# Kernel optimization log

Measured on AMD Instinct MI355X. Metric: run time of the kernel, lower is better.

Reference implementation:

```python
import jax, jax.numpy as jnp
import numpy as np

M_FUZZ = 2.0        # self.m
EPSILON = 1e-8      # self.Epsilon
MAX_ITER = 25       # self.max_iterion


def setup_inputs() -> dict:
    key = jax.random.key(0)
    k1, k2 = jax.random.split(key)
    data = jax.random.normal(k1, (300000, 64), dtype=jnp.float32)
    u0_raw = jax.random.uniform(k2, (300000, 64), dtype=jnp.float32)
    return {"data": data, "u0_raw": u0_raw, "cluster": 64}


def reference(data, u0_raw, cluster):
    # Fuzzy c-means, faithful to GranularComputing.forward:
    #   iterate: C = center(U); U = update(U, C); C_new = center(U);
    #            stop if ||C_new - C||_F < Epsilon; return C (pre-update center).
    m = M_FUZZ
    p = 2.0 / (m - 1.0)  # exponent in membership update (== 2.0)
    N, D = data.shape

    # initialize_matrix_U: random rows normalized to sum to 1
    U0 = u0_raw / jnp.sum(u0_raw, axis=1, keepdims=True)  # [N, c]

    def center(U):
        Um = U ** m                                        # [N, c]
        num = Um.T @ data                                  # [c, D]
        den = jnp.sum(Um, axis=0)[:, None]                 # [c, 1]
        return num / den

    x2 = jnp.sum(data * data, axis=1, keepdims=True)       # [N, 1]

    def sqdist(C):
        # squared Euclidean distances [N, c] via expansion (no N x c x D tensor)
        c2 = jnp.sum(C * C, axis=1)                        # [c]
        return jnp.maximum(x2 + c2 - 2.0 * (data @ C.T), 0.0)

    def step(carry, _):
        U, C_ret, done = carry
        C = center(U)                                      # [c, D]
        # u_ij = 1 / sum_k (d_ij / d_ik)^p  ==  d_ij^{-p} / sum_k d_ik^{-p}
        w = sqdist(C) ** (-p / 2.0)                        # [N, c]
        U_new = w / jnp.sum(w, axis=1, keepdims=True)
        C_new = center(U_new)
        diff = jnp.sqrt(jnp.sum((C_new - C) ** 2))
        # freeze state after convergence (emulates the early break)
        U_out = jnp.where(done, U, U_new)
        C_out = jnp.where(done, C_ret, C)
        return (U_out, C_out, done | (diff < EPSILON)), None

    C0 = jnp.zeros((cluster, D), dtype=data.dtype)
    (_, V, _), _ = jax.lax.scan(
        step, (U0, C0, jnp.array(False)), None, length=MAX_ITER + 1
    )
    return V  # [cluster, D]
```

## Files before the change

kernel.cpp:

```cpp
#include <hip/hip_runtime.h>


#define DM 64
#define CL 64
#define PARTIAL_STRIDE 4160
#define MAX_ITER 25
#define MAX_BLOCKS 768
#define LDP 72

typedef __attribute__((ext_vector_type(8))) short bf16x8;
typedef __attribute__((ext_vector_type(4))) float f32x4;

__device__ __forceinline__ unsigned f2bf1(float f) {
  unsigned u = __builtin_bit_cast(unsigned, f);
  return (u + 0x7FFFu + ((u >> 16) & 1u)) >> 16;
}
__device__ __forceinline__ unsigned pkbf(float a, float b) {
  return f2bf1(a) | (f2bf1(b) << 16);
}
__device__ __forceinline__ unsigned cvtpk_bf16(float a, float b) {
  unsigned r;
  asm("v_cvt_pk_bf16_f32 %0, %1, %2" : "=v"(r) : "v"(a), "v"(b));
  return r;
}

__device__ __forceinline__ float wave_sum(float v) {
#define DPPADD(ctrl, rmask)                                                  \
  v += __builtin_bit_cast(float, __builtin_amdgcn_update_dpp(                \
           0, __builtin_bit_cast(int, v), ctrl, rmask, 0xf, false));
  DPPADD(0x111, 0xf)
  DPPADD(0x112, 0xf)
  DPPADD(0x114, 0xf)
  DPPADD(0x118, 0xf)
  DPPADD(0x142, 0xa)
  DPPADD(0x143, 0xc)
#undef DPPADD
  return __builtin_bit_cast(
      float, __builtin_amdgcn_readlane(__builtin_bit_cast(int, v), 63));
}

__device__ __forceinline__ float group16_sum(float v) {
#define DPPADD(ctrl)                                                         \
  v += __builtin_bit_cast(float, __builtin_amdgcn_update_dpp(                \
           0, __builtin_bit_cast(int, v), ctrl, 0xf, 0xf, false));
  DPPADD(0xB1)
  DPPADD(0x4E)
  DPPADD(0x141)
  DPPADD(0x140)
#undef DPPADD
  return v;
}

__global__ __launch_bounds__(256)
void fcm_prep(const float* __restrict__ data, float* __restrict__ x2,
              unsigned short* __restrict__ xbf,
              float* __restrict__ diffac, int* __restrict__ done,
              int* __restrict__ ticket, int N) {
  size_t i = (size_t)blockIdx.x * blockDim.x + threadIdx.x;
  if (i == 0) { *diffac = 0.0f; *done = 0; *ticket = 0; }
  size_t nvec = (size_t)N * (DM / 4);
  if (i >= nvec) return;
  float4 v = ((const float4*)data)[i];
  float s = fmaf(v.x, v.x, fmaf(v.y, v.y, fmaf(v.z, v.z, v.w * v.w)));
  float rs = group16_sum(s);
  if ((threadIdx.x & 15) == 0) x2[i >> 4] = rs;
  uint2 pk = {cvtpk_bf16(v.x, v.y), cvtpk_bf16(v.z, v.w)};
  ((uint2*)xbf)[i] = pk;
}

template <bool INIT>
__global__ __launch_bounds__(256, 3)
void fcm_pass(const unsigned short* __restrict__ xbf, const float* __restrict__ x2,
              const float* __restrict__ CU,
              float* __restrict__ partial, const int* __restrict__ done,
              int N, int ntiles) {
  if (!INIT && *done) return;
  __shared__ __align__(16) unsigned short Xb[64 * LDP];
  __shared__ __align__(16) unsigned short XTb[64 * LDP];
  __shared__ __align__(16) unsigned short umT[64 * LDP];
  __shared__ __align__(16) float x2s[64];

  const int tid  = threadIdx.x;
  const int w    = __builtin_amdgcn_readfirstlane(tid >> 6);
  const int col  = tid & 15;
  const int quad = (tid >> 4) & 3;

  bf16x8 cf0[4], cf1[4];
  float c2v[4];
  if (!INIT) {
#pragma unroll
    for (int jt = 0; jt < 4; jt++) {
      const float* crow = CU + (size_t)(16 * jt + col) * DM;
      float4 ca = *(const float4*)(crow + quad * 8);
      float4 cb = *(const float4*)(crow + quad * 8 + 4);
      float4 cc = *(const float4*)(crow + 32 + quad * 8);
      float4 cd = *(const float4*)(crow + 32 + quad * 8 + 4);
      float cp = ca.x*ca.x + ca.y*ca.y + ca.z*ca.z + ca.w*ca.w
               + cb.x*cb.x + cb.y*cb.y + cb.z*cb.z + cb.w*cb.w
               + cc.x*cc.x + cc.y*cc.y + cc.z*cc.z + cc.w*cc.w
               + cd.x*cd.x + cd.y*cd.y + cd.z*cd.z + cd.w*cd.w;
      cp += __shfl_xor(cp, 16, 64);
      cp += __shfl_xor(cp, 32, 64);
      c2v[jt] = cp;
      union { bf16x8 v; unsigned u[4]; } P0, P1;
      P0.u[0] = pkbf(ca.x, ca.y); P0.u[1] = pkbf(ca.z, ca.w);
      P0.u[2] = pkbf(cb.x, cb.y); P0.u[3] = pkbf(cb.z, cb.w);
      P1.u[0] = pkbf(cc.x, cc.y); P1.u[1] = pkbf(cc.z, cc.w);
      P1.u[2] = pkbf(cd.x, cd.y); P1.u[3] = pkbf(cd.z, cd.w);
      cf0[jt] = P0.v; cf1[jt] = P1.v;
    }
  }

  union { bf16x8 v; unsigned u[4]; } ON;
  ON.u[0] = ON.u[1] = ON.u[2] = ON.u[3] = 0x3F803F80u;
  const bf16x8 onesf = ON.v;

  f32x4 D2[4];
#pragma unroll
  for (int dt = 0; dt < 4; dt++) D2[dt] = f32x4{0.f, 0.f, 0.f, 0.f};
  f32x4 Dden = f32x4{0.f, 0.f, 0.f, 0.f};

  const int sp  = tid & 63;
  const int sd0 = (tid >> 6) * 8;
  const unsigned short* gsrc = xbf + (size_t)sp * DM + sd0;
  unsigned short* xw = &Xb[sp * LDP + sd0];
  unsigned short* xt = &XTb[sd0 * LDP + sp];

  for (int t = blockIdx.x; t < ntiles; t += gridDim.x) {
    const int base = t * 64;
    const int np = min(64, N - base);
    __syncthreads();

    {
      bf16x8 v0 = {0, 0, 0, 0, 0, 0, 0, 0};
      bf16x8 v1 = {0, 0, 0, 0, 0, 0, 0, 0};
      if (sp < np) {
        const unsigned short* g = gsrc + (size_t)base * DM;
        v0 = *(const bf16x8*)(g);
        v1 = *(const bf16x8*)(g + 32);
      }
      *(bf16x8*)(void*)xw = v0;
      *(bf16x8*)(void*)(xw + 32) = v1;
#pragma unroll
      for (int k = 0; k < 8; k++) xt[k * LDP] = (unsigned short)v0[k];
#pragma unroll
      for (int k = 0; k < 8; k++) xt[(k + 32) * LDP] = (unsigned short)v1[k];
    }
    if (tid < 64) x2s[tid] = (base + tid < N) ? x2[base + tid] : 0.0f;
    __syncthreads();

    float Wv[4][4];
    if (INIT) {
#pragma unroll
      for (int jt = 0; jt < 4; jt++)
#pragma unroll
        for (int r = 0; r < 4; r++) {
          int pl = 16 * w + quad * 4 + r;
          Wv[jt][r] = (pl < np)
              ? CU[(size_t)(base + pl) * CL + 16 * jt + col] : 0.0f;
        }
    } else {
      bf16x8 a0 = *(const bf16x8*)(const void*)&Xb[(16 * w + col) * LDP + quad * 8];
      bf16x8 a1 = *(const bf16x8*)(const void*)&Xb[(16 * w + col) * LDP + 32 + quad * 8];
      f32x4 x2p = *(const f32x4*)(const void*)&x2s[16 * w + quad * 4];
#pragma unroll
      for (int jt = 0; jt < 4; jt++) {
        f32x4 s = f32x4{0.f, 0.f, 0.f, 0.f};
        s = __builtin_amdgcn_mfma_f32_16x16x32_bf16(a0, cf0[jt], s, 0, 0, 0);
        s = __builtin_amdgcn_mfma_f32_16x16x32_bf16(a1, cf1[jt], s, 0, 0, 0);
#pragma unroll
        for (int r = 0; r < 4; r++) {
          float dist = fmaxf(fmaf(-2.0f, s[r], x2p[r] + c2v[jt]), 0.0f);
          Wv[jt][r] = __builtin_amdgcn_rcpf(dist);
        }
      }
    }

    float rr[4];
#pragma unroll
    for (int r = 0; r < 4; r++) {
      float rs = Wv[0][r] + Wv[1][r] + Wv[2][r] + Wv[3][r];
      rs = group16_sum(rs);
      int pl = 16 * w + quad * 4 + r;
      rr[r] = (pl < np) ? __builtin_amdgcn_rcpf(rs) : 0.0f;
    }

#pragma unroll
    for (int jt = 0; jt < 4; jt++) {
      float u0v = Wv[jt][0] * rr[0], u1v = Wv[jt][1] * rr[1];
      float u2v = Wv[jt][2] * rr[2], u3v = Wv[jt][3] * rr[3];
      uint2 pk = {cvtpk_bf16(u0v * u0v, u1v * u1v),
                  cvtpk_bf16(u2v * u2v, u3v * u3v)};
      *(uint2*)(void*)&umT[(16 * jt + col) * LDP + 16 * w + quad * 4] = pk;
    }
    __syncthreads();

#pragma unroll
    for (int pb = 0; pb < 2; pb++) {
      bf16x8 au = *(const bf16x8*)(const void*)&umT[(16 * w + col) * LDP + pb * 32 + quad * 8];
      Dden = __builtin_amdgcn_mfma_f32_16x16x32_bf16(au, onesf, Dden, 0, 0, 0);
#pragma unroll
      for (int dt = 0; dt < 4; dt++) {
        bf16x8 bx = *(const bf16x8*)(const void*)&XTb[(dt * 16 + col) * LDP + pb * 32 + quad * 8];
        D2[dt] = __builtin_amdgcn_mfma_f32_16x16x32_bf16(au, bx, D2[dt], 0, 0, 0);
      }
    }
  }

  float* pbuf = partial + (size_t)blockIdx.x * PARTIAL_STRIDE;
  if (col == 0) {
    float4 dv = {Dden[0], Dden[1], Dden[2], Dden[3]};
    *(float4*)(void*)&pbuf[CL * DM + 16 * w + quad * 4] = dv;
  }
#pragma unroll
  for (int dt = 0; dt < 4; dt++)
#pragma unroll
    for (int r = 0; r < 4; r++)
      pbuf[(size_t)(16 * w + quad * 4 + r) * DM + dt * 16 + col] = D2[dt][r];
}

__global__ __launch_bounds__(1024, 1)
void fcm_reduce(const float* __restrict__ partial, float* __restrict__ Cnew,
                const float* __restrict__ Cold, float* __restrict__ out,
                float* __restrict__ diffac, int* __restrict__ done,
                int* __restrict__ ticket, int compute_diff, int nb) {
  if (compute_diff && *done) return;
  __shared__ float sm[16 * 64];
  __shared__ float sden[1024];
  __shared__ int lastflag;
  __shared__ float sdiff;
  int j = blockIdx.x;
  int tid = threadIdx.x;
  int d = tid & 63;
  int slice = tid >> 6;
  float s = 0.0f;
  for (int b = slice; b < nb; b += 16)
    s += partial[(size_t)b * PARTIAL_STRIDE + j * DM + d];
  sm[slice * 64 + d] = s;
  float dv = 0.0f;
  for (int b = tid; b < nb; b += 1024)
    dv += partial[(size_t)b * PARTIAL_STRIDE + CL * DM + j];
  sden[tid] = dv;
  __syncthreads();
#pragma unroll
  for (int st = 8; st; st >>= 1) {
    if (slice < st) sm[slice * 64 + d] += sm[(slice + st) * 64 + d];
    __syncthreads();
  }
#pragma unroll
  for (int st = 512; st >= 64; st >>= 1) {
    if (tid < st) sden[tid] += sden[tid + st];
    __syncthreads();
  }
  if (tid < 64) {
    float denj = wave_sum(sden[tid]);
    float c = sm[tid] / denj;
    Cnew[j * DM + tid] = c;
    if (compute_diff) {
      float df = c - Cold[j * DM + tid];
      float tot = wave_sum(df * df);
      if (tid == 0) atomicAdd(diffac, tot);
    }
  }
  if (!compute_diff) return;
  __syncthreads();
  if (tid == 0) {
    __threadfence();
    int t = atomicAdd(ticket, 1);
    lastflag = (t == (int)gridDim.x - 1);
  }
  __syncthreads();
  if (!lastflag) return;
  if (tid == 0) sdiff = atomicAdd(diffac, 0.0f);
  __syncthreads();
  if (sdiff < 1e-16f) {
    for (int i = tid; i < CL * DM; i += 1024) out[i] = Cold[i];
    if (tid == 0) *done = 1;
  }
  if (tid == 0) { *diffac = 0.0f; *ticket = 0; }
}

__global__ void fcm_final(const float* __restrict__ Clast, float* __restrict__ out,
                          const int* __restrict__ done) {
  if (*done) return;
  int i = blockIdx.x * blockDim.x + threadIdx.x;
  if (i < CL * DM) out[i] = Clast[i];
}

extern "C" void kernel_launch(void* const* d_in, const int* in_sizes, int n_in,
                              void* d_out, int out_size, void* d_ws, size_t ws_size,
                              hipStream_t stream) {
  const float* data = (const float*)d_in[0];
  const float* u0   = (const float*)d_in[1];
  float* out = (float*)d_out;
  int N = in_sizes[0] / DM;
  int ntiles = (N + 63) / 64;

  float* ws = (float*)d_ws;
  size_t Noff = ((size_t)N + 15) & ~(size_t)15;
  float* x2 = ws;
  unsigned short* xbf = (unsigned short*)(ws + Noff);
  float* C0 = ws + Noff + (size_t)N * 32;
  float* C1 = C0 + CL * DM;
  float* diffac = C1 + CL * DM;
  int* done = (int*)(diffac + 1);
  int* ticket = (int*)(diffac + 2);
  float* partial = diffac + 16;

  size_t used = Noff + (size_t)N * 32 + 2 * CL * DM + 16;
  size_t avail = (ws_size / 4 > used) ? (ws_size / 4 - used) / PARTIAL_STRIDE : 0;
  int nb = (int)(avail < MAX_BLOCKS ? avail : MAX_BLOCKS);
  if (nb < 1) nb = 1;

  size_t nvec = (size_t)N * (DM / 4);
  hipLaunchKernelGGL(fcm_prep, dim3((unsigned)((nvec + 255) / 256)), dim3(256), 0,
                     stream, data, x2, xbf, diffac, done, ticket, N);
  hipLaunchKernelGGL((fcm_pass<true>), dim3(nb), dim3(256), 0, stream,
                     xbf, x2, u0, partial, done, N, ntiles);
  hipLaunchKernelGGL(fcm_reduce, dim3(64), dim3(1024), 0, stream,
                     partial, C0, C1, out, diffac, done, ticket, 0, nb);

  float* bufs[2] = {C0, C1};
  for (int k = 0; k < MAX_ITER; k++) {
    float* Cc = bufs[k & 1];
    float* Cn = bufs[(k + 1) & 1];
    hipLaunchKernelGGL((fcm_pass<false>), dim3(nb), dim3(256), 0, stream,
                       xbf, x2, Cc, partial, done, N, ntiles);
    hipLaunchKernelGGL(fcm_reduce, dim3(64), dim3(1024), 0, stream,
                       partial, Cn, Cc, out, diffac, done, ticket, 1, nb);
  }
  hipLaunchKernelGGL(fcm_final, dim3(16), dim3(256), 0, stream,
                     bufs[1], out, done);
}
```

Baseline: 387.6 us.

## Software-pipeline tile loads and split center reduction across four blocks per cluster

The pass kernel now double-buffers the X tiles in LDS and prefetches the next tile's bf16 rows and x2 values into registers. The second GEMM for the previous tile is deferred so it overlaps with staging the current tile, which removes one barrier per tile. The reduce kernel is split into 256 blocks of 256 threads, four per cluster. Each block reduces a quarter of the partials and combines them through global atomics with a per-cluster ticket, plus a global ticket for the convergence check. This adds LDS use, which may lower occupancy, and relies on atomic accumulation and self-resetting counters.

```diff
diff --git a/kernel.cpp b/kernel.cpp
--- a/kernel.cpp
+++ b/kernel.cpp
@@ -7,6 +7,7 @@
 #define MAX_ITER 25
 #define MAX_BLOCKS 768
 #define LDP 72
+#define ZACC_SZ 4224
 
 typedef __attribute__((ext_vector_type(8))) short bf16x8;
 typedef __attribute__((ext_vector_type(4))) float f32x4;
@@ -53,11 +54,12 @@
 
 __global__ __launch_bounds__(256)
 void fcm_prep(const float* __restrict__ data, float* __restrict__ x2,
-              unsigned short* __restrict__ xbf,
+              unsigned short* __restrict__ xbf, float* __restrict__ zacc,
               float* __restrict__ diffac, int* __restrict__ done,
               int* __restrict__ ticket, int N) {
   size_t i = (size_t)blockIdx.x * blockDim.x + threadIdx.x;
   if (i == 0) { *diffac = 0.0f; *done = 0; *ticket = 0; }
+  if (i < ZACC_SZ) zacc[i] = 0.0f;
   size_t nvec = (size_t)N * (DM / 4);
   if (i >= nvec) return;
   float4 v = ((const float4*)data)[i];
@@ -75,10 +77,10 @@
               float* __restrict__ partial, const int* __restrict__ done,
               int N, int ntiles) {
   if (!INIT && *done) return;
-  __shared__ __align__(16) unsigned short Xb[64 * LDP];
-  __shared__ __align__(16) unsigned short XTb[64 * LDP];
+  __shared__ __align__(16) unsigned short Xb[2][64 * LDP];
+  __shared__ __align__(16) unsigned short XTb[2][64 * LDP];
   __shared__ __align__(16) unsigned short umT[64 * LDP];
-  __shared__ __align__(16) float x2s[64];
+  __shared__ __align__(16) float x2s[2][64];
 
   const int tid  = threadIdx.x;
   const int w    = __builtin_amdgcn_readfirstlane(tid >> 6);
@@ -123,30 +125,70 @@
   const int sp  = tid & 63;
   const int sd0 = (tid >> 6) * 8;
   const unsigned short* gsrc = xbf + (size_t)sp * DM + sd0;
-  unsigned short* xw = &Xb[sp * LDP + sd0];
-  unsigned short* xt = &XTb[sd0 * LDP + sp];
-
-  for (int t = blockIdx.x; t < ntiles; t += gridDim.x) {
+
+  auto do_gemm2 = [&](int cb) {
+#pragma unroll
+    for (int pb = 0; pb < 2; pb++) {
+      bf16x8 au = *(const bf16x8*)(const void*)&umT[(16 * w + col) * LDP + pb * 32 + quad * 8];
+      Dden = __builtin_amdgcn_mfma_f32_16x16x32_bf16(au, onesf, Dden, 0, 0, 0);
+#pragma unroll
+      for (int dt = 0; dt < 4; dt++) {
+        bf16x8 bx = *(const bf16x8*)(const void*)&XTb[cb][(dt * 16 + col) * LDP + pb * 32 + quad * 8];
+        D2[dt] = __builtin_amdgcn_mfma_f32_16x16x32_bf16(au, bx, D2[dt], 0, 0, 0);
+      }
+    }
+  };
+
+  bf16x8 rv0 = {0, 0, 0, 0, 0, 0, 0, 0};
+  bf16x8 rv1 = {0, 0, 0, 0, 0, 0, 0, 0};
+  float rx2 = 0.0f;
+  {
+    int t0 = blockIdx.x;
+    if (t0 < ntiles) {
+      int base = t0 * 64;
+      int np = min(64, N - base);
+      if (sp < np) {
+        const unsigned short* g = gsrc + (size_t)base * DM;
+        rv0 = *(const bf16x8*)(g);
+        rv1 = *(const bf16x8*)(g + 32);
+      }
+      if (tid < 64 && base + tid < N) rx2 = x2[base + tid];
+    }
+  }
+
+  int c = 0;
+  int it = 0;
+  for (int t = blockIdx.x; t < ntiles; t += gridDim.x, ++it) {
     const int base = t * 64;
     const int np = min(64, N - base);
     __syncthreads();
 
+    if (it > 0) do_gemm2(c ^ 1);
+
+    *(bf16x8*)(void*)&Xb[c][sp * LDP + sd0] = rv0;
+    *(bf16x8*)(void*)&Xb[c][sp * LDP + sd0 + 32] = rv1;
+#pragma unroll
+    for (int k = 0; k < 8; k++) XTb[c][(sd0 + k) * LDP + sp] = (unsigned short)rv0[k];
+#pragma unroll
+    for (int k = 0; k < 8; k++) XTb[c][(sd0 + 32 + k) * LDP + sp] = (unsigned short)rv1[k];
+    if (tid < 64) x2s[c][tid] = rx2;
+
     {
-      bf16x8 v0 = {0, 0, 0, 0, 0, 0, 0, 0};
-      bf16x8 v1 = {0, 0, 0, 0, 0, 0, 0, 0};
-      if (sp < np) {
-        const unsigned short* g = gsrc + (size_t)base * DM;
-        v0 = *(const bf16x8*)(g);
-        v1 = *(const bf16x8*)(g + 32);
+      int tn = t + gridDim.x;
+      rv0 = bf16x8{0, 0, 0, 0, 0, 0, 0, 0};
+      rv1 = bf16x8{0, 0, 0, 0, 0, 0, 0, 0};
+      rx2 = 0.0f;
+      if (tn < ntiles) {
+        int nbase = tn * 64;
+        int nnp = min(64, N - nbase);
+        if (sp < nnp) {
+          const unsigned short* g = gsrc + (size_t)nbase * DM;
+          rv0 = *(const bf16x8*)(g);
+          rv1 = *(const bf16x8*)(g + 32);
+        }
+        if (tid < 64 && nbase + tid < N) rx2 = x2[nbase + tid];
       }
-      *(bf16x8*)(void*)xw = v0;
-      *(bf16x8*)(void*)(xw + 32) = v1;
-#pragma unroll
-      for (int k = 0; k < 8; k++) xt[k * LDP] = (unsigned short)v0[k];
-#pragma unroll
-      for (int k = 0; k < 8; k++) xt[(k + 32) * LDP] = (unsigned short)v1[k];
-    }
-    if (tid < 64) x2s[tid] = (base + tid < N) ? x2[base + tid] : 0.0f;
+    }
     __syncthreads();
 
     float Wv[4][4];
@@ -160,9 +202,9 @@
               ? CU[(size_t)(base + pl) * CL + 16 * jt + col] : 0.0f;
         }
     } else {
-      bf16x8 a0 = *(const bf16x8*)(const void*)&Xb[(16 * w + col) * LDP + quad * 8];
-      bf16x8 a1 = *(const bf16x8*)(const void*)&Xb[(16 * w + col) * LDP + 32 + quad * 8];
-      f32x4 x2p = *(const f32x4*)(const void*)&x2s[16 * w + quad * 4];
+      bf16x8 a0 = *(const bf16x8*)(const void*)&Xb[c][(16 * w + col) * LDP + quad * 8];
+      bf16x8 a1 = *(const bf16x8*)(const void*)&Xb[c][(16 * w + col) * LDP + 32 + quad * 8];
+      f32x4 x2p = *(const f32x4*)(const void*)&x2s[c][16 * w + quad * 4];
 #pragma unroll
       for (int jt = 0; jt < 4; jt++) {
         f32x4 s = f32x4{0.f, 0.f, 0.f, 0.f};
@@ -193,18 +235,12 @@
                   cvtpk_bf16(u2v * u2v, u3v * u3v)};
       *(uint2*)(void*)&umT[(16 * jt + col) * LDP + 16 * w + quad * 4] = pk;
     }
+    c ^= 1;
+  }
+
+  if (it > 0) {
     __syncthreads();
-
-#pragma unroll
-    for (int pb = 0; pb < 2; pb++) {
-      bf16x8 au = *(const bf16x8*)(const void*)&umT[(16 * w + col) * LDP + pb * 32 + quad * 8];
-      Dden = __builtin_amdgcn_mfma_f32_16x16x32_bf16(au, onesf, Dden, 0, 0, 0);
-#pragma unroll
-      for (int dt = 0; dt < 4; dt++) {
-        bf16x8 bx = *(const bf16x8*)(const void*)&XTb[(dt * 16 + col) * LDP + pb * 32 + quad * 8];
-        D2[dt] = __builtin_amdgcn_mfma_f32_16x16x32_bf16(au, bx, D2[dt], 0, 0, 0);
-      }
-    }
+    do_gemm2(c ^ 1);
   }
 
   float* pbuf = partial + (size_t)blockIdx.x * PARTIAL_STRIDE;
@@ -219,62 +255,69 @@
       pbuf[(size_t)(16 * w + quad * 4 + r) * DM + dt * 16 + col] = D2[dt][r];
 }
 
-__global__ __launch_bounds__(1024, 1)
+__global__ __launch_bounds__(256)
 void fcm_reduce(const float* __restrict__ partial, float* __restrict__ Cnew,
                 const float* __restrict__ Cold, float* __restrict__ out,
+                float* __restrict__ Cacc, float* __restrict__ Dacc,
+                int* __restrict__ jtick,
                 float* __restrict__ diffac, int* __restrict__ done,
                 int* __restrict__ ticket, int compute_diff, int nb) {
   if (compute_diff && *done) return;
-  __shared__ float sm[16 * 64];
-  __shared__ float sden[1024];
+  __shared__ float red[4][64];
   __shared__ int lastflag;
-  __shared__ float sdiff;
-  int j = blockIdx.x;
-  int tid = threadIdx.x;
-  int d = tid & 63;
-  int slice = tid >> 6;
+  __shared__ float sdv;
+  const int tid = threadIdx.x;
+  const int j = blockIdx.x >> 2;
+  const int q = blockIdx.x & 3;
+  const int nbq = nb >> 2;
+  const int i0 = q * nbq;
+  const int iend = (q == 3) ? nb : i0 + nbq;
+  const int d = tid & 63;
+  const int slice = tid >> 6;
+
   float s = 0.0f;
-  for (int b = slice; b < nb; b += 16)
-    s += partial[(size_t)b * PARTIAL_STRIDE + j * DM + d];
-  sm[slice * 64 + d] = s;
-  float dv = 0.0f;
-  for (int b = tid; b < nb; b += 1024)
-    dv += partial[(size_t)b * PARTIAL_STRIDE + CL * DM + j];
-  sden[tid] = dv;
-  __syncthreads();
-#pragma unroll
-  for (int st = 8; st; st >>= 1) {
-    if (slice < st) sm[slice * 64 + d] += sm[(slice + st) * 64 + d];
-    __syncthreads();
-  }
-#pragma unroll
-  for (int st = 512; st >= 64; st >>= 1) {
-    if (tid < st) sden[tid] += sden[tid + st];
-    __syncthreads();
-  }
+  for (int i = i0 + slice; i < iend; i += 4)
+    s += partial[(size_t)i * PARTIAL_STRIDE + j * DM + d];
+  red[slice][d] = s;
+  __syncthreads();
   if (tid < 64) {
-    float denj = wave_sum(sden[tid]);
-    float c = sm[tid] / denj;
-    Cnew[j * DM + tid] = c;
+    float ss = red[0][d] + red[1][d] + red[2][d] + red[3][d];
+    atomicAdd(&Cacc[j * DM + d], ss);
+    float dv = 0.0f;
+    for (int i = i0 + d; i < iend; i += 64)
+      dv += partial[(size_t)i * PARTIAL_STRIDE + CL * DM + j];
+    float dsum = wave_sum(dv);
+    if (tid == 0) atomicAdd(&Dacc[j], dsum);
+  }
+  __threadfence();
+  if (tid == 0) lastflag = (atomicAdd(&jtick[j], 1) == 3);
+  __syncthreads();
+  if (!lastflag) return;
+
+  float tot = 0.0f;
+  if (tid < 64) {
+    float n = atomicAdd(&Cacc[j * DM + tid], 0.0f);
+    float dn = atomicAdd(&Dacc[j], 0.0f);
+    float cval = n / dn;
+    Cnew[j * DM + tid] = cval;
     if (compute_diff) {
-      float df = c - Cold[j * DM + tid];
-      float tot = wave_sum(df * df);
+      float df = cval - Cold[j * DM + tid];
+      tot = wave_sum(df * df);
       if (tid == 0) atomicAdd(diffac, tot);
     }
-  }
-  if (!compute_diff) return;
-  __syncthreads();
-  if (tid == 0) {
-    __threadfence();
-    int t = atomicAdd(ticket, 1);
-    lastflag = (t == (int)gridDim.x - 1);
-  }
+    Cacc[j * DM + tid] = 0.0f;
+    if (tid == 0) { Dacc[j] = 0.0f; jtick[j] = 0; }
+  }
+  __threadfence();
+  __syncthreads();
+  if (tid == 0) lastflag = (atomicAdd(ticket, 1) == CL - 1);
   __syncthreads();
   if (!lastflag) return;
-  if (tid == 0) sdiff = atomicAdd(diffac, 0.0f);
-  __syncthreads();
-  if (sdiff < 1e-16f) {
-    for (int i = tid; i < CL * DM; i += 1024) out[i] = Cold[i];
+
+  if (tid == 0) sdv = atomicAdd(diffac, 0.0f);
+  __syncthreads();
+  if (compute_diff && sdv < 1e-16f) {
+    for (int i = tid; i < CL * DM; i += 256) out[i] = Cold[i];
     if (tid == 0) *done = 1;
   }
   if (tid == 0) { *diffac = 0.0f; *ticket = 0; }
@@ -305,20 +348,25 @@
   float* diffac = C1 + CL * DM;
   int* done = (int*)(diffac + 1);
   int* ticket = (int*)(diffac + 2);
-  float* partial = diffac + 16;
-
-  size_t used = Noff + (size_t)N * 32 + 2 * CL * DM + 16;
+  float* zacc = diffac + 16;
+  float* Cacc = zacc;
+  float* Dacc = zacc + CL * DM;
+  int* jtick = (int*)(zacc + CL * DM + CL);
+  float* partial = zacc + ZACC_SZ;
+
+  size_t used = Noff + (size_t)N * 32 + 2 * CL * DM + 16 + ZACC_SZ;
   size_t avail = (ws_size / 4 > used) ? (ws_size / 4 - used) / PARTIAL_STRIDE : 0;
   int nb = (int)(avail < MAX_BLOCKS ? avail : MAX_BLOCKS);
-  if (nb < 1) nb = 1;
+  if (nb < 4) nb = 4;
 
   size_t nvec = (size_t)N * (DM / 4);
   hipLaunchKernelGGL(fcm_prep, dim3((unsigned)((nvec + 255) / 256)), dim3(256), 0,
-                     stream, data, x2, xbf, diffac, done, ticket, N);
+                     stream, data, x2, xbf, zacc, diffac, done, ticket, N);
   hipLaunchKernelGGL((fcm_pass<true>), dim3(nb), dim3(256), 0, stream,
                      xbf, x2, u0, partial, done, N, ntiles);
-  hipLaunchKernelGGL(fcm_reduce, dim3(64), dim3(1024), 0, stream,
-                     partial, C0, C1, out, diffac, done, ticket, 0, nb);
+  hipLaunchKernelGGL(fcm_reduce, dim3(256), dim3(256), 0, stream,
+                     partial, C0, C1, out, Cacc, Dacc, jtick,
+                     diffac, done, ticket, 0, nb);
 
   float* bufs[2] = {C0, C1};
   for (int k = 0; k < MAX_ITER; k++) {
@@ -326,8 +374,9 @@
     float* Cn = bufs[(k + 1) & 1];
     hipLaunchKernelGGL((fcm_pass<false>), dim3(nb), dim3(256), 0, stream,
                        xbf, x2, Cc, partial, done, N, ntiles);
-    hipLaunchKernelGGL(fcm_reduce, dim3(64), dim3(1024), 0, stream,
-                       partial, Cn, Cc, out, diffac, done, ticket, 1, nb);
+    hipLaunchKernelGGL(fcm_reduce, dim3(256), dim3(256), 0, stream,
+                       partial, Cn, Cc, out, Cacc, Dacc, jtick,
+                       diffac, done, ticket, 1, nb);
   }
   hipLaunchKernelGGL(fcm_final, dim3(16), dim3(256), 0, stream,
                      bufs[1], out, done);
```

New measurement: 469.6 us. +21.2%, slower.

## Double-buffer X tiles and prefetch next tile into registers in fcm_pass

Applied to the files above, without the earlier changes.

Double-buffers the shared-memory X, transposed X and x2 tiles and issues the global loads for the next tile into registers before the current tile's distance/membership work. The second GEMM (U^m^T X accumulation) for the previous tile is deferred into the next iteration, which removes one __syncthreads per tile and overlaps global load latency with compute. In exchange it roughly doubles LDS use for X tiles, which may lower occupancy under the 3-blocks-per-CU launch bound, and it increases register pressure.

```diff
diff --git a/kernel.cpp b/kernel.cpp
--- a/kernel.cpp
+++ b/kernel.cpp
@@ -75,10 +75,10 @@
               float* __restrict__ partial, const int* __restrict__ done,
               int N, int ntiles) {
   if (!INIT && *done) return;
-  __shared__ __align__(16) unsigned short Xb[64 * LDP];
-  __shared__ __align__(16) unsigned short XTb[64 * LDP];
+  __shared__ __align__(16) unsigned short Xb[2][64 * LDP];
+  __shared__ __align__(16) unsigned short XTb[2][64 * LDP];
   __shared__ __align__(16) unsigned short umT[64 * LDP];
-  __shared__ __align__(16) float x2s[64];
+  __shared__ __align__(16) float x2s[2][64];
 
   const int tid  = threadIdx.x;
   const int w    = __builtin_amdgcn_readfirstlane(tid >> 6);
@@ -123,30 +123,70 @@
   const int sp  = tid & 63;
   const int sd0 = (tid >> 6) * 8;
   const unsigned short* gsrc = xbf + (size_t)sp * DM + sd0;
-  unsigned short* xw = &Xb[sp * LDP + sd0];
-  unsigned short* xt = &XTb[sd0 * LDP + sp];
-
-  for (int t = blockIdx.x; t < ntiles; t += gridDim.x) {
+
+  auto do_gemm2 = [&](int cb) {
+#pragma unroll
+    for (int pb = 0; pb < 2; pb++) {
+      bf16x8 au = *(const bf16x8*)(const void*)&umT[(16 * w + col) * LDP + pb * 32 + quad * 8];
+      Dden = __builtin_amdgcn_mfma_f32_16x16x32_bf16(au, onesf, Dden, 0, 0, 0);
+#pragma unroll
+      for (int dt = 0; dt < 4; dt++) {
+        bf16x8 bx = *(const bf16x8*)(const void*)&XTb[cb][(dt * 16 + col) * LDP + pb * 32 + quad * 8];
+        D2[dt] = __builtin_amdgcn_mfma_f32_16x16x32_bf16(au, bx, D2[dt], 0, 0, 0);
+      }
+    }
+  };
+
+  bf16x8 rv0 = {0, 0, 0, 0, 0, 0, 0, 0};
+  bf16x8 rv1 = {0, 0, 0, 0, 0, 0, 0, 0};
+  float rx2 = 0.0f;
+  {
+    int t0 = blockIdx.x;
+    if (t0 < ntiles) {
+      int base = t0 * 64;
+      int np = min(64, N - base);
+      if (sp < np) {
+        const unsigned short* g = gsrc + (size_t)base * DM;
+        rv0 = *(const bf16x8*)(g);
+        rv1 = *(const bf16x8*)(g + 32);
+      }
+      if (tid < 64 && base + tid < N) rx2 = x2[base + tid];
+    }
+  }
+
+  int c = 0;
+  int it = 0;
+  for (int t = blockIdx.x; t < ntiles; t += gridDim.x, ++it) {
     const int base = t * 64;
     const int np = min(64, N - base);
     __syncthreads();
 
+    if (it > 0) do_gemm2(c ^ 1);
+
+    *(bf16x8*)(void*)&Xb[c][sp * LDP + sd0] = rv0;
+    *(bf16x8*)(void*)&Xb[c][sp * LDP + sd0 + 32] = rv1;
+#pragma unroll
+    for (int k = 0; k < 8; k++) XTb[c][(sd0 + k) * LDP + sp] = (unsigned short)rv0[k];
+#pragma unroll
+    for (int k = 0; k < 8; k++) XTb[c][(sd0 + 32 + k) * LDP + sp] = (unsigned short)rv1[k];
+    if (tid < 64) x2s[c][tid] = rx2;
+
     {
-      bf16x8 v0 = {0, 0, 0, 0, 0, 0, 0, 0};
-      bf16x8 v1 = {0, 0, 0, 0, 0, 0, 0, 0};
-      if (sp < np) {
-        const unsigned short* g = gsrc + (size_t)base * DM;
-        v0 = *(const bf16x8*)(g);
-        v1 = *(const bf16x8*)(g + 32);
+      int tn = t + gridDim.x;
+      rv0 = bf16x8{0, 0, 0, 0, 0, 0, 0, 0};
+      rv1 = bf16x8{0, 0, 0, 0, 0, 0, 0, 0};
+      rx2 = 0.0f;
+      if (tn < ntiles) {
+        int nbase = tn * 64;
+        int nnp = min(64, N - nbase);
+        if (sp < nnp) {
+          const unsigned short* g = gsrc + (size_t)nbase * DM;
+          rv0 = *(const bf16x8*)(g);
+          rv1 = *(const bf16x8*)(g + 32);
+        }
+        if (tid < 64 && nbase + tid < N) rx2 = x2[nbase + tid];
       }
-      *(bf16x8*)(void*)xw = v0;
-      *(bf16x8*)(void*)(xw + 32) = v1;
-#pragma unroll
-      for (int k = 0; k < 8; k++) xt[k * LDP] = (unsigned short)v0[k];
-#pragma unroll
-      for (int k = 0; k < 8; k++) xt[(k + 32) * LDP] = (unsigned short)v1[k];
-    }
-    if (tid < 64) x2s[tid] = (base + tid < N) ? x2[base + tid] : 0.0f;
+    }
     __syncthreads();
 
     float Wv[4][4];
@@ -160,9 +200,9 @@
               ? CU[(size_t)(base + pl) * CL + 16 * jt + col] : 0.0f;
         }
     } else {
-      bf16x8 a0 = *(const bf16x8*)(const void*)&Xb[(16 * w + col) * LDP + quad * 8];
-      bf16x8 a1 = *(const bf16x8*)(const void*)&Xb[(16 * w + col) * LDP + 32 + quad * 8];
-      f32x4 x2p = *(const f32x4*)(const void*)&x2s[16 * w + quad * 4];
+      bf16x8 a0 = *(const bf16x8*)(const void*)&Xb[c][(16 * w + col) * LDP + quad * 8];
+      bf16x8 a1 = *(const bf16x8*)(const void*)&Xb[c][(16 * w + col) * LDP + 32 + quad * 8];
+      f32x4 x2p = *(const f32x4*)(const void*)&x2s[c][16 * w + quad * 4];
 #pragma unroll
       for (int jt = 0; jt < 4; jt++) {
         f32x4 s = f32x4{0.f, 0.f, 0.f, 0.f};
@@ -193,18 +233,12 @@
                   cvtpk_bf16(u2v * u2v, u3v * u3v)};
       *(uint2*)(void*)&umT[(16 * jt + col) * LDP + 16 * w + quad * 4] = pk;
     }
-    __syncthreads();
-
-#pragma unroll
-    for (int pb = 0; pb < 2; pb++) {
-      bf16x8 au = *(const bf16x8*)(const void*)&umT[(16 * w + col) * LDP + pb * 32 + quad * 8];
-      Dden = __builtin_amdgcn_mfma_f32_16x16x32_bf16(au, onesf, Dden, 0, 0, 0);
-#pragma unroll
-      for (int dt = 0; dt < 4; dt++) {
-        bf16x8 bx = *(const bf16x8*)(const void*)&XTb[(dt * 16 + col) * LDP + pb * 32 + quad * 8];
-        D2[dt] = __builtin_amdgcn_mfma_f32_16x16x32_bf16(au, bx, D2[dt], 0, 0, 0);
-      }
-    }
+    c ^= 1;
+  }
+
+  if (it > 0) {
+    __syncthreads();
+    do_gemm2(c ^ 1);
   }
 
   float* pbuf = partial + (size_t)blockIdx.x * PARTIAL_STRIDE;
```

New measurement: 379.0 us. 2.2% less time.
